# Optimization experiments

Hardware: AMD Instinct MI355X
Metric: run time of the kernel (lower is better)

The kernel has to match this reference:

```python
import jax, jax.numpy as jnp
import numpy as np

DIM = 2048
N_HEADS = 16
N_KV_HEADS = 4
HEAD_DIM = DIM // N_HEADS  # 128
N_REP = N_HEADS // N_KV_HEADS  # 4
SEQ = 2048
BATCH = 2


def apply_rope(x, cos, sin):
    # x: [b, s, h, d]; cos/sin: [s, d//2]
    xr = x[..., 0::2]
    xi = x[..., 1::2]
    c = cos[None, :, None, :]
    s = sin[None, :, None, :]
    out_r = xr * c - xi * s
    out_i = xr * s + xi * c
    # interleave back: stack on last axis then flatten
    out = jnp.stack([out_r, out_i], axis=-1)
    return out.reshape(x.shape)


def setup_inputs() -> dict:
    key = jax.random.key(0)
    ks = jax.random.split(key, 7)
    x = jax.random.normal(ks[0], (BATCH, SEQ, DIM), dtype=jnp.float32)
    # realistic rotary tables
    inv_freq = 1.0 / (10000.0 ** (np.arange(0, HEAD_DIM, 2, dtype=np.float32) / HEAD_DIM))
    t = np.arange(SEQ, dtype=np.float32)
    freqs = np.outer(t, inv_freq)  # [S, d//2]
    freqs_cos = jnp.asarray(np.cos(freqs))
    freqs_sin = jnp.asarray(np.sin(freqs))
    sc = 0.02
    Wq = jax.random.normal(ks[1], (DIM, N_HEADS * HEAD_DIM), dtype=jnp.float32) * sc
    Wk = jax.random.normal(ks[2], (DIM, N_KV_HEADS * HEAD_DIM), dtype=jnp.float32) * sc
    Wv = jax.random.normal(ks[3], (DIM, N_KV_HEADS * HEAD_DIM), dtype=jnp.float32) * sc
    Wo = jax.random.normal(ks[4], (N_HEADS * HEAD_DIM, DIM), dtype=jnp.float32) * sc
    return {"x": x, "freqs_cos": freqs_cos, "freqs_sin": freqs_sin,
            "Wq": Wq, "Wk": Wk, "Wv": Wv, "Wo": Wo}


def reference(x, freqs_cos, freqs_sin, Wq, Wk, Wv, Wo):
    b, s, _ = x.shape
    xq = (x @ Wq).reshape(b, s, N_HEADS, HEAD_DIM)
    xk = (x @ Wk).reshape(b, s, N_KV_HEADS, HEAD_DIM)
    xv = (x @ Wv).reshape(b, s, N_KV_HEADS, HEAD_DIM)
    xq = apply_rope(xq, freqs_cos, freqs_sin)
    xk = apply_rope(xk, freqs_cos, freqs_sin)
    # GQA attention without materializing repeated KV:
    # group query heads as [b, g, r, s, d] with g=N_KV_HEADS, r=N_REP
    q = xq.reshape(b, s, N_KV_HEADS, N_REP, HEAD_DIM)
    scale = 1.0 / jnp.sqrt(jnp.float32(HEAD_DIM))
    scores = jnp.einsum('bqgrd,bkgd->bgrqk', q, xk) * scale  # [b,g,r,s,s]
    causal = jnp.tril(jnp.ones((s, s), dtype=bool))
    scores = jnp.where(causal[None, None, None], scores, jnp.finfo(scores.dtype).min)
    probs = jax.nn.softmax(scores, axis=-1)
    out = jnp.einsum('bgrqk,bkgd->bqgrd', probs, xv)  # [b,s,g,r,d]
    out = out.reshape(b, s, N_HEADS * HEAD_DIM)
    return out @ Wo
```

## Files before the change

kernel.cpp:

```cpp
#include <hip/hip_runtime.h>
#include <stdint.h>
#include <stddef.h>

constexpr int BATCH = 2;
constexpr int SEQ   = 2048;
constexpr int EMB   = 2048;
constexpr int HEADS = 16;
constexpr int GQA   = 4;
constexpr int HDIM  = 128;
constexpr int NQKV  = 3072;
constexpr int VOFF  = 2560;
constexpr int MROWS = BATCH * SEQ;

typedef _Float16 half8  __attribute__((ext_vector_type(8)));
typedef _Float16 half4v __attribute__((ext_vector_type(4)));
typedef float    floatx4 __attribute__((ext_vector_type(4)));

__device__ __forceinline__ void st_c(float* p, float v)    { *p = v; }
__device__ __forceinline__ void st_c(_Float16* p, float v) { *p = (_Float16)v; }

__device__ __forceinline__ void gld16(const _Float16* g, _Float16* l) {
    __builtin_amdgcn_global_load_lds(
        (const __attribute__((address_space(1))) void*)g,
        (__attribute__((address_space(3))) void*)l, 16, 0, 0);
}

__global__ void cast_x_kernel(const float* __restrict__ x, _Float16* __restrict__ xh) {
    int i = (blockIdx.x * 256 + threadIdx.x) * 4;
    float4 v = *(const float4*)(x + i);
    half4v h;
    h[0] = (_Float16)v.x; h[1] = (_Float16)v.y; h[2] = (_Float16)v.z; h[3] = (_Float16)v.w;
    *(half4v*)(xh + i) = h;
}

__global__ void transpose_cast(const float* __restrict__ in, _Float16* __restrict__ out,
                               int R, int C) {
    __shared__ float tile[32][33];
    int cb = blockIdx.x * 32, rb = blockIdx.y * 32;
    int tx = threadIdx.x, ty = threadIdx.y;
    #pragma unroll
    for (int j = 0; j < 32; j += 8)
        tile[ty + j][tx] = in[(size_t)(rb + ty + j) * C + (cb + tx)];
    __syncthreads();
    #pragma unroll
    for (int j = 0; j < 32; j += 8)
        out[(size_t)(cb + ty + j) * R + (rb + tx)] = (_Float16)tile[tx][ty + j];
}

template <typename CT, bool ROPE>
__global__ __launch_bounds__(256) void gemm_bt(const _Float16* __restrict__ A,
                                               const _Float16* __restrict__ Bt,
                                               CT* __restrict__ C,
                                               int M, int N, int K,
                                               const float* __restrict__ fc,
                                               const float* __restrict__ fs) {
    constexpr int LDT = 40;
    __shared__ _Float16 As[128 * LDT];
    __shared__ _Float16 Bs[128 * LDT];
    const int tid  = threadIdx.x;
    const int bm   = blockIdx.y * 128, bn = blockIdx.x * 128;
    const int lane = tid & 63, wid = tid >> 6;
    const int wr   = wid >> 1, wc = wid & 1;
    const int qd   = lane >> 4, m15 = lane & 15;

    const int sr = tid >> 2;
    const int sc = (tid & 3) * 8;
    const _Float16* Ag  = A  + (size_t)(bm + sr) * K + sc;
    const _Float16* Ag2 = Ag + (size_t)64 * K;
    const _Float16* Bg  = Bt + (size_t)(bn + sr) * K + sc;
    const _Float16* Bg2 = Bg + (size_t)64 * K;

    half8 a0 = *(const half8*)(Ag);
    half8 a1 = *(const half8*)(Ag2);
    half8 b0 = *(const half8*)(Bg);
    half8 b1 = *(const half8*)(Bg2);

    floatx4 acc[4][4] = {};

    _Float16* AsW  = As + sr * LDT + sc;
    _Float16* AsW2 = AsW + 64 * LDT;
    _Float16* BsW  = Bs + sr * LDT + sc;
    _Float16* BsW2 = BsW + 64 * LDT;
    const _Float16* AsR = As + (wr * 64 + m15) * LDT + qd * 8;
    const _Float16* BsR = Bs + (wc * 64 + m15) * LDT + qd * 8;

    for (int k0 = 0; k0 < K; k0 += 32) {
        *(half8*)AsW  = a0;  *(half8*)AsW2 = a1;
        *(half8*)BsW  = b0;  *(half8*)BsW2 = b1;
        __syncthreads();
        if (k0 + 32 < K) {
            a0 = *(const half8*)(Ag  + k0 + 32);
            a1 = *(const half8*)(Ag2 + k0 + 32);
            b0 = *(const half8*)(Bg  + k0 + 32);
            b1 = *(const half8*)(Bg2 + k0 + 32);
        }
        half8 af[4], bf[4];
        #pragma unroll
        for (int i = 0; i < 4; i++) af[i] = *(const half8*)(AsR + i * 16 * LDT);
        #pragma unroll
        for (int i = 0; i < 4; i++) bf[i] = *(const half8*)(BsR + i * 16 * LDT);
        #pragma unroll
        for (int mi = 0; mi < 4; mi++)
            #pragma unroll
            for (int ni = 0; ni < 4; ni++)
                acc[mi][ni] = __builtin_amdgcn_mfma_f32_16x16x32_f16(af[mi], bf[ni], acc[mi][ni], 0, 0, 0);
        __syncthreads();
    }

    #pragma unroll
    for (int mi = 0; mi < 4; mi++)
        #pragma unroll
        for (int ni = 0; ni < 4; ni++)
            #pragma unroll
            for (int r = 0; r < 4; r++) {
                int row = bm + wr * 64 + mi * 16 + qd * 4 + r;
                int col = bn + wc * 64 + ni * 16 + m15;
                float v = acc[mi][ni][r];
                if (ROPE && col < VOFF) {
                    int si = row & (SEQ - 1);
                    int fi = (col >> 1) & 63;
                    float c  = fc[si * 64 + fi];
                    float sn = fs[si * 64 + fi];
                    float other = __shfl_xor(v, 1, 64);
                    v = (m15 & 1) ? (v * c + other * sn) : (v * c - other * sn);
                }
                st_c(&C[(size_t)row * N + col], v);
            }
}

__global__ void transpose_v(const _Float16* __restrict__ qkv, _Float16* __restrict__ vt) {
    __shared__ _Float16 tile[32][33];
    int sb = blockIdx.x * 32, db = blockIdx.y * 32;
    int bg = blockIdx.z;
    int tx = threadIdx.x, ty = threadIdx.y;
    const _Float16* src = qkv + (size_t)(bg >> 2) * SEQ * NQKV + VOFF + (bg & 3) * HDIM;
    #pragma unroll
    for (int j = 0; j < 32; j += 8)
        tile[ty + j][tx] = src[(size_t)(sb + ty + j) * NQKV + db + tx];
    __syncthreads();
    _Float16* dst = vt + (size_t)bg * HDIM * SEQ;
    #pragma unroll
    for (int j = 0; j < 32; j += 8)
        dst[(size_t)(db + ty + j) * SEQ + sb + tx] = tile[tx][ty + j];
}

__global__ __launch_bounds__(512, 2) void flash_attn(const _Float16* __restrict__ qkv,
                                                     const _Float16* __restrict__ vt,
                                                     _Float16* __restrict__ ob) {
    const int bx   = blockIdx.x;
    const int g    = blockIdx.y;
    const int b    = blockIdx.z;
    const int tid  = threadIdx.x;
    const int lane = tid & 63, wid = tid >> 6;
    const int h    = g * 4 + (wid & 3);
    const int su   = wid >> 2;
    const int qd   = lane >> 4, m15 = lane & 15;

    __shared__ _Float16 Ks[2][64 * 128];
    __shared__ _Float16 Vs[2][128 * 64];
    __shared__ _Float16 Ps[8][16 * 64];

    const _Float16* kg = qkv + (size_t)(b * SEQ) * NQKV + EMB + g * HDIM;
    const _Float16* vg = vt + (size_t)(b * GQA + g) * HDIM * SEQ;
    _Float16* pw = Ps[wid];

    const int kl = lane >> 4, kc16 = lane & 15;
    const int vl = lane >> 3, vc8  = lane & 7;
    const _Float16* kgp[2]; const _Float16* vgp[2];
    int ksoff[2], vsoff[2];
    #pragma unroll
    for (int j = 0; j < 2; j++) {
        int t = wid * 2 + j;
        int kr = t * 4 + kl;
        kgp[j] = kg + (size_t)kr * NQKV + ((kc16 ^ (kr & 15)) * 8);
        ksoff[j] = t * 512;
        int vr = t * 8 + vl;
        vgp[j] = vg + (size_t)vr * SEQ + ((vc8 ^ (vr & 7)) * 8);
        vsoff[j] = t * 512;
    }

    half8 ones;
    #pragma unroll
    for (int i = 0; i < 8; i++) ones[i] = (_Float16)1.0f;
    const _Float16 qsc = (_Float16)(0.08838834764831845f * 1.44269504088896341f);

    for (int ph = 0; ph < 2; ++ph) {
        const int sidx   = ph ? bx : 63 - bx;
        const int q0     = sidx * 32;
        const int ktLast = sidx >> 1;

        __syncthreads();
        #pragma unroll
        for (int j = 0; j < 2; j++) gld16(kgp[j], &Ks[0][ksoff[j]]);
        #pragma unroll
        for (int j = 0; j < 2; j++) gld16(vgp[j], &Vs[0][vsoff[j]]);

        half8 qf[4];
        {
            const _Float16* qb = qkv + (size_t)(b * SEQ + q0 + su * 16 + m15) * NQKV + h * HDIM + qd * 8;
            #pragma unroll
            for (int kc = 0; kc < 4; kc++) {
                half8 q = *(const half8*)(qb + kc * 32);
                #pragma unroll
                for (int i = 0; i < 8; i++) q[i] = (_Float16)(q[i] * qsc);
                qf[kc] = q;
            }
        }

        floatx4 o[9] = {};

        for (int kt = 0; kt <= ktLast; ++kt) {
            const int cur = kt & 1;
            __syncthreads();
            if (kt < ktLast) {
                const int nb = cur ^ 1;
                const size_t ko = (size_t)(kt + 1) * 64;
                #pragma unroll
                for (int j = 0; j < 2; j++) gld16(kgp[j] + ko * NQKV, &Ks[nb][ksoff[j]]);
                #pragma unroll
                for (int j = 0; j < 2; j++) gld16(vgp[j] + ko, &Vs[nb][vsoff[j]]);
            }
            const _Float16* ksb = Ks[cur];
            const _Float16* vsb = Vs[cur];

            floatx4 sa[4] = {};
            #pragma unroll
            for (int nt = 0; nt < 4; ++nt) {
                const int kr = nt * 16 + m15;
                #pragma unroll
                for (int kc = 0; kc < 4; ++kc) {
                    half8 kf = *(const half8*)(&ksb[kr * 128 + (((kc * 4 + qd) ^ (kr & 15)) * 8)]);
                    sa[nt] = __builtin_amdgcn_mfma_f32_16x16x32_f16(qf[kc], kf, sa[nt], 0, 0, 0);
                }
            }

            const bool diag = (kt == ktLast);
            const int  k0   = kt * 64;
            #pragma unroll
            for (int r = 0; r < 4; r++) {
                const int prow = qd * 4 + r;
                const int rowg = q0 + su * 16 + prow;
                #pragma unroll
                for (int nt = 0; nt < 4; nt++) {
                    float p = __builtin_exp2f(sa[nt][r]);
                    if (diag && (k0 + nt * 16 + m15 > rowg)) p = 0.f;
                    int chunk = (nt * 2 + (m15 >> 3)) ^ (prow & 7);
                    pw[prow * 64 + chunk * 8 + (m15 & 7)] = (_Float16)p;
                }
            }

            half8 pf[2];
            #pragma unroll
            for (int kc = 0; kc < 2; kc++)
                pf[kc] = *(const half8*)(&pw[m15 * 64 + (((kc * 4 + qd) ^ (m15 & 7)) * 8)]);

            #pragma unroll
            for (int dt = 0; dt < 8; dt++) {
                const int vr = dt * 16 + m15;
                #pragma unroll
                for (int kc = 0; kc < 2; kc++) {
                    half8 vf = *(const half8*)(&vsb[vr * 64 + (((kc * 4 + qd) ^ (vr & 7)) * 8)]);
                    o[dt] = __builtin_amdgcn_mfma_f32_16x16x32_f16(pf[kc], vf, o[dt], 0, 0, 0);
                }
            }
            o[8] = __builtin_amdgcn_mfma_f32_16x16x32_f16(pf[0], ones, o[8], 0, 0, 0);
            o[8] = __builtin_amdgcn_mfma_f32_16x16x32_f16(pf[1], ones, o[8], 0, 0, 0);
        }

        float linv[4];
        #pragma unroll
        for (int r = 0; r < 4; r++) linv[r] = 1.0f / o[8][r];
        _Float16* od = ob + (size_t)(b * SEQ + q0 + su * 16) * EMB + h * HDIM;
        #pragma unroll
        for (int dt = 0; dt < 8; dt++)
            #pragma unroll
            for (int r = 0; r < 4; r++)
                od[(size_t)(qd * 4 + r) * EMB + dt * 16 + m15] = (_Float16)(o[dt][r] * linv[r]);
    }
}

extern "C" void kernel_launch(void* const* d_in, const int* in_sizes, int n_in,
                              void* d_out, int out_size, void* d_ws, size_t ws_size,
                              hipStream_t stream) {
    (void)in_sizes; (void)n_in; (void)out_size; (void)ws_size;
    const float* x  = (const float*)d_in[0];
    const float* fc = (const float*)d_in[1];
    const float* fs = (const float*)d_in[2];
    const float* Wq = (const float*)d_in[3];
    const float* Wk = (const float*)d_in[4];
    const float* Wv = (const float*)d_in[5];
    const float* Wo = (const float*)d_in[6];
    float* out = (float*)d_out;

    _Float16* Xb   = (_Float16*)d_ws;
    _Float16* Wqkv = Xb   + (size_t)MROWS * EMB;
    _Float16* WoT  = Wqkv + (size_t)NQKV * EMB;
    _Float16* C1   = WoT  + (size_t)EMB * EMB;
    _Float16* Vt   = Wqkv;
    _Float16* Ob   = Xb;

    dim3 tb(32, 8);
    cast_x_kernel<<<MROWS * EMB / 1024, 256, 0, stream>>>(x, Xb);
    transpose_cast<<<dim3(EMB / 32, EMB / 32), tb, 0, stream>>>(Wq, Wqkv, EMB, EMB);
    transpose_cast<<<dim3(512 / 32, EMB / 32), tb, 0, stream>>>(Wk, Wqkv + (size_t)EMB * EMB, EMB, 512);
    transpose_cast<<<dim3(512 / 32, EMB / 32), tb, 0, stream>>>(Wv, Wqkv + (size_t)VOFF * EMB, EMB, 512);
    transpose_cast<<<dim3(EMB / 32, EMB / 32), tb, 0, stream>>>(Wo, WoT, EMB, EMB);

    gemm_bt<_Float16, true><<<dim3(NQKV / 128, MROWS / 128), 256, 0, stream>>>(
        Xb, Wqkv, C1, MROWS, NQKV, EMB, fc, fs);
    transpose_v<<<dim3(SEQ / 32, HDIM / 32, BATCH * GQA), tb, 0, stream>>>(C1, Vt);
    flash_attn<<<dim3(32, GQA, BATCH), 512, 0, stream>>>(C1, Vt, Ob);
    gemm_bt<float, false><<<dim3(EMB / 128, MROWS / 128), 256, 0, stream>>>(
        Ob, WoT, out, MROWS, EMB, EMB, nullptr, nullptr);
}
```

Measured before the change: 325.4 us.

## Load GEMM tiles directly into LDS and raise wave priority around attention MFMAs

The projection GEMM drops its register-staged prefetch and padded shared-memory tiles. It now issues global_load_lds transfers straight into unpadded 128x32 LDS tiles each k-step, which removes the VGPR staging and the ds_write instructions. The cost is that global loads no longer overlap the previous tile's MFMAs, and the unpadded 64-byte row stride may cause LDS bank conflicts on fragment reads. In the attention kernel, s_setprio brackets the QK and PV MFMA blocks so waves in their matrix phases get issue priority over waves doing softmax work.

```diff
diff --git a/kernel.cpp b/kernel.cpp
--- a/kernel.cpp
+++ b/kernel.cpp
@@ -54,51 +54,38 @@
                                                int M, int N, int K,
                                                const float* __restrict__ fc,
                                                const float* __restrict__ fs) {
-    constexpr int LDT = 40;
-    __shared__ _Float16 As[128 * LDT];
-    __shared__ _Float16 Bs[128 * LDT];
+    __shared__ _Float16 As[128 * 32];
+    __shared__ _Float16 Bs[128 * 32];
     const int tid  = threadIdx.x;
     const int bm   = blockIdx.y * 128, bn = blockIdx.x * 128;
     const int lane = tid & 63, wid = tid >> 6;
     const int wr   = wid >> 1, wc = wid & 1;
     const int qd   = lane >> 4, m15 = lane & 15;
 
-    const int sr = tid >> 2;
-    const int sc = (tid & 3) * 8;
-    const _Float16* Ag  = A  + (size_t)(bm + sr) * K + sc;
-    const _Float16* Ag2 = Ag + (size_t)64 * K;
-    const _Float16* Bg  = Bt + (size_t)(bn + sr) * K + sc;
-    const _Float16* Bg2 = Bg + (size_t)64 * K;
-
-    half8 a0 = *(const half8*)(Ag);
-    half8 a1 = *(const half8*)(Ag2);
-    half8 b0 = *(const half8*)(Bg);
-    half8 b1 = *(const half8*)(Bg2);
+    const int srow = lane >> 2;
+    const int scol = (lane & 3) * 8;
+    const _Float16* Ag = A  + (size_t)(bm + wid * 16 + srow) * K + scol;
+    const _Float16* Bg = Bt + (size_t)(bn + wid * 16 + srow) * K + scol;
+    const size_t rowskip = (size_t)64 * K;
+    _Float16* AsW = As + wid * 16 * 32;
+    _Float16* BsW = Bs + wid * 16 * 32;
+
+    const _Float16* AsR = As + (wr * 64 + m15) * 32 + qd * 8;
+    const _Float16* BsR = Bs + (wc * 64 + m15) * 32 + qd * 8;
 
     floatx4 acc[4][4] = {};
 
-    _Float16* AsW  = As + sr * LDT + sc;
-    _Float16* AsW2 = AsW + 64 * LDT;
-    _Float16* BsW  = Bs + sr * LDT + sc;
-    _Float16* BsW2 = BsW + 64 * LDT;
-    const _Float16* AsR = As + (wr * 64 + m15) * LDT + qd * 8;
-    const _Float16* BsR = Bs + (wc * 64 + m15) * LDT + qd * 8;
-
     for (int k0 = 0; k0 < K; k0 += 32) {
-        *(half8*)AsW  = a0;  *(half8*)AsW2 = a1;
-        *(half8*)BsW  = b0;  *(half8*)BsW2 = b1;
+        gld16(Ag + k0,           AsW);
+        gld16(Ag + rowskip + k0, AsW + 64 * 32);
+        gld16(Bg + k0,           BsW);
+        gld16(Bg + rowskip + k0, BsW + 64 * 32);
         __syncthreads();
-        if (k0 + 32 < K) {
-            a0 = *(const half8*)(Ag  + k0 + 32);
-            a1 = *(const half8*)(Ag2 + k0 + 32);
-            b0 = *(const half8*)(Bg  + k0 + 32);
-            b1 = *(const half8*)(Bg2 + k0 + 32);
-        }
         half8 af[4], bf[4];
         #pragma unroll
-        for (int i = 0; i < 4; i++) af[i] = *(const half8*)(AsR + i * 16 * LDT);
-        #pragma unroll
-        for (int i = 0; i < 4; i++) bf[i] = *(const half8*)(BsR + i * 16 * LDT);
+        for (int i = 0; i < 4; i++) af[i] = *(const half8*)(AsR + i * 16 * 32);
+        #pragma unroll
+        for (int i = 0; i < 4; i++) bf[i] = *(const half8*)(BsR + i * 16 * 32);
         #pragma unroll
         for (int mi = 0; mi < 4; mi++)
             #pragma unroll
@@ -224,6 +211,7 @@
             const _Float16* vsb = Vs[cur];
 
             floatx4 sa[4] = {};
+            __builtin_amdgcn_s_setprio(1);
             #pragma unroll
             for (int nt = 0; nt < 4; ++nt) {
                 const int kr = nt * 16 + m15;
@@ -233,6 +221,7 @@
                     sa[nt] = __builtin_amdgcn_mfma_f32_16x16x32_f16(qf[kc], kf, sa[nt], 0, 0, 0);
                 }
             }
+            __builtin_amdgcn_s_setprio(0);
 
             const bool diag = (kt == ktLast);
             const int  k0   = kt * 64;
@@ -254,6 +243,7 @@
             for (int kc = 0; kc < 2; kc++)
                 pf[kc] = *(const half8*)(&pw[m15 * 64 + (((kc * 4 + qd) ^ (m15 & 7)) * 8)]);
 
+            __builtin_amdgcn_s_setprio(1);
             #pragma unroll
             for (int dt = 0; dt < 8; dt++) {
                 const int vr = dt * 16 + m15;
@@ -265,6 +255,7 @@
             }
             o[8] = __builtin_amdgcn_mfma_f32_16x16x32_f16(pf[0], ones, o[8], 0, 0, 0);
             o[8] = __builtin_amdgcn_mfma_f32_16x16x32_f16(pf[1], ones, o[8], 0, 0, 0);
+            __builtin_amdgcn_s_setprio(0);
         }
 
         float linv[4];
```

Result: slower. 339.7 us (+4.4%).
